# Kernel tuning notes

Measured on AMD Instinct MI355X. Metric: run time of the kernel, lower is better.

The kernel has to match this reference:

```python
import jax, jax.numpy as jnp
import numpy as np

B, T, E, H = 2, 2048, 1024, 16
D = E // H  # head_dim = 64


def setup_inputs() -> dict:
    key = jax.random.key(0)
    ks = jax.random.split(key, 9)
    s = 0.02
    x = jax.random.normal(ks[0], (B, T, E), dtype=jnp.float32)
    # additive causal mask, broadcastable to (B, H, T, T)
    causal = jnp.tril(jnp.ones((T, T), dtype=bool))
    uni_causal_mask = jnp.where(causal, 0.0, -1e9).astype(jnp.float32)[None, None]
    # torch Linear weights are (out_features, in_features); out = H*D, in = D
    Wq = jax.random.normal(ks[1], (H * D, D), dtype=jnp.float32) * s
    bq = jax.random.normal(ks[2], (H * D,), dtype=jnp.float32) * s
    Wk = jax.random.normal(ks[3], (H * D, D), dtype=jnp.float32) * s
    bk = jax.random.normal(ks[4], (H * D,), dtype=jnp.float32) * s
    Wv = jax.random.normal(ks[5], (H * D, D), dtype=jnp.float32) * s
    bv = jax.random.normal(ks[6], (H * D,), dtype=jnp.float32) * s
    Wp = jax.random.normal(ks[7], (E, E), dtype=jnp.float32) * s
    bp = jax.random.normal(ks[8], (E,), dtype=jnp.float32) * s
    return {"x": x, "uni_causal_mask": uni_causal_mask,
            "Wq": Wq, "bq": bq, "Wk": Wk, "bk": bk,
            "Wv": Wv, "bv": bv, "Wp": Wp, "bp": bp}


def _per_head_proj(xh, W, b):
    # xh: (B, T, H, D). Original code projects each head's D-dim slice with
    # Linear(D, H*D) and get_head_dim keeps only the diagonal block i for
    # head i, i.e. each head uses W[i*D:(i+1)*D, :] and b[i*D:(i+1)*D].
    W3 = W.reshape(H, D, D)  # (H, out D, in D)
    b2 = b.reshape(H, D)
    y = jnp.einsum('bthi,hoi->bhto', xh, W3) + b2[None, :, None, :]
    return y  # (B, H, T, D)


def reference(x, uni_causal_mask, Wq, bq, Wk, bk, Wv, bv, Wp, bp):
    b, t, e = x.shape
    xh = x.reshape(b, t, H, D)
    q = _per_head_proj(xh, Wq, bq)  # (B,H,T,D)
    k = _per_head_proj(xh, Wk, bk)
    v = _per_head_proj(xh, Wv, bv)
    scale = D ** (-0.5)
    attn = jnp.einsum('bhtd,bhsd->bhts', (q * scale).astype(jnp.float32),
                      k.astype(jnp.float32))
    attn = attn + uni_causal_mask
    attn = jax.nn.softmax(attn, axis=-1).astype(x.dtype)
    out = jnp.einsum('bhts,bhsd->bhtd', attn, v)
    out = out.transpose(0, 2, 1, 3).reshape(b, t, e)
    return out @ Wp.T + bp
```

## Files before the change

kernel.cpp:

```cpp
#include <hip/hip_runtime.h>

typedef __attribute__((ext_vector_type(4))) float f32x4;
typedef __attribute__((ext_vector_type(8))) __bf16 bf16x8;
typedef __attribute__((ext_vector_type(4))) unsigned short us4;
typedef __attribute__((ext_vector_type(8))) unsigned short us8;

#define DEVI static __device__ __forceinline__

constexpr int T_ = 2048, E_ = 1024, H_ = 16, D_ = 64;
#define QSCALE (0.125f * 1.44269504088896f)

DEVI unsigned short f2b(float f) {
  union { __bf16 b; unsigned short u; } c; c.b = (__bf16)f; return c.u;
}

DEVI unsigned pkw(float a, float b) {
  union { __bf16 h[2]; unsigned u; } c;
  c.h[0] = (__bf16)a; c.h[1] = (__bf16)b; return c.u;
}

#if __has_builtin(__builtin_amdgcn_exp2f)
DEVI float fexp2(float x) { return __builtin_amdgcn_exp2f(x); }
#else
DEVI float fexp2(float x) { return __expf(x * 0.69314718056f); }
#endif

DEVI f32x4 mfma16(bf16x8 a, bf16x8 b, f32x4 c) {
  return __builtin_amdgcn_mfma_f32_16x16x32_bf16(a, b, c, 0, 0, 0);
}

__launch_bounds__(256)
__global__ void wcvt_kernel(const float* __restrict__ Wq,
                            const float* __restrict__ Wk,
                            const float* __restrict__ Wv,
                            unsigned short* __restrict__ wqb,
                            unsigned short* __restrict__ wkb,
                            unsigned short* __restrict__ wvb)
{
  int blk = blockIdx.x;
  const float* src; unsigned short* dst; float s = 1.0f;
  if (blk < 64)       { src = Wq; dst = wqb; s = QSCALE; }
  else if (blk < 128) { src = Wk; dst = wkb; blk -= 64; }
  else                { src = Wv; dst = wvb; blk -= 128; }
  int i = blk * 256 + threadIdx.x;
  float4 v = *(const float4*)(src + (size_t)i * 4);
  us4 o; o[0] = f2b(v.x * s); o[1] = f2b(v.y * s); o[2] = f2b(v.z * s); o[3] = f2b(v.w * s);
  *(us4*)(dst + (size_t)i * 4) = o;
}

__launch_bounds__(256)
__global__ void wpcvt_kernel(const float* __restrict__ Wp,
                             unsigned short* __restrict__ wpb)
{
  int i = blockIdx.x * 256 + threadIdx.x;
  float4 v = *(const float4*)(Wp + (size_t)i * 4);
  us4 o; o[0] = f2b(v.x); o[1] = f2b(v.y); o[2] = f2b(v.z); o[3] = f2b(v.w);
  *(us4*)(wpb + (size_t)i * 4) = o;
}

__launch_bounds__(256)
__global__ void qkv_kernel(const float* __restrict__ x,
                           const unsigned short* __restrict__ wqb,
                           const float* __restrict__ bq,
                           const unsigned short* __restrict__ wkb,
                           const float* __restrict__ bk,
                           const unsigned short* __restrict__ wvb,
                           const float* __restrict__ bv,
                           unsigned short* __restrict__ qo,
                           unsigned short* __restrict__ ko,
                           unsigned short* __restrict__ vto)
{
  const int bh = blockIdx.x;
  const int b  = bh >> 4;
  const int h  = bh & (H_ - 1);
  const int t0 = blockIdx.y * 128;
  __shared__ unsigned short Xl[128][72];
  __shared__ unsigned short Wl[3][64][72];
  const int tid = threadIdx.x;

  #pragma unroll
  for (int p = 0; p < 8; ++p) {
    int idx = p * 256 + tid;
    int row = idx >> 4, c4 = idx & 15;
    float4 v = *(const float4*)(x + ((size_t)(b * T_ + t0 + row)) * E_ + h * 64 + c4 * 4);
    us4 o; o[0] = f2b(v.x); o[1] = f2b(v.y); o[2] = f2b(v.z); o[3] = f2b(v.w);
    *(us4*)&Xl[row][c4 * 4] = o;
  }
  {
    const unsigned short* wsrc0 = wqb + (size_t)h * 4096;
    const unsigned short* wsrc1 = wkb + (size_t)h * 4096;
    const unsigned short* wsrc2 = wvb + (size_t)h * 4096;
    #pragma unroll
    for (int p = 0; p < 2; ++p) {
      int idx = p * 256 + tid;
      int row = idx >> 3, c8 = (idx & 7) * 8;
      *(us8*)&Wl[0][row][c8] = *(const us8*)(wsrc0 + row * 64 + c8);
      *(us8*)&Wl[1][row][c8] = *(const us8*)(wsrc1 + row * 64 + c8);
      *(us8*)&Wl[2][row][c8] = *(const us8*)(wsrc2 + row * 64 + c8);
    }
  }
  __syncthreads();

  const int w = tid >> 6, lane = tid & 63, lo = lane & 15, g = lane >> 4;
  const int tl0 = w * 32;

  bf16x8 xb[2][2];
  #pragma unroll
  for (int tt = 0; tt < 2; ++tt)
    #pragma unroll
    for (int kd = 0; kd < 2; ++kd)
      xb[tt][kd] = *(const bf16x8*)&Xl[tl0 + tt * 16 + lo][kd * 32 + g * 8];

  #pragma unroll
  for (int tsel = 0; tsel < 2; ++tsel) {
    const float* bias = tsel ? bk : bq;
    unsigned short* outp = tsel ? ko : qo;
    const float bs = tsel ? 1.0f : QSCALE;
    #pragma unroll
    for (int ot = 0; ot < 4; ++ot) {
      bf16x8 a0 = *(const bf16x8*)&Wl[tsel][ot * 16 + lo][g * 8];
      bf16x8 a1 = *(const bf16x8*)&Wl[tsel][ot * 16 + lo][32 + g * 8];
      float4 bv4 = *(const float4*)(bias + h * 64 + ot * 16 + g * 4);
      float bb[4] = {bv4.x * bs, bv4.y * bs, bv4.z * bs, bv4.w * bs};
      #pragma unroll
      for (int tt = 0; tt < 2; ++tt) {
        f32x4 acc = {0.f, 0.f, 0.f, 0.f};
        acc = mfma16(a0, xb[tt][0], acc);
        acc = mfma16(a1, xb[tt][1], acc);
        int tg = t0 + tl0 + tt * 16 + lo;
        us4 pk;
        #pragma unroll
        for (int r = 0; r < 4; ++r) pk[r] = f2b(acc[r] + bb[r]);
        *(us4*)(outp + ((size_t)(bh * T_ + tg)) * 64 + ot * 16 + g * 4) = pk;
      }
    }
  }

  #pragma unroll
  for (int rt = 0; rt < 2; ++rt) {
    bf16x8 a0 = *(const bf16x8*)&Xl[tl0 + rt * 16 + lo][g * 8];
    bf16x8 a1 = *(const bf16x8*)&Xl[tl0 + rt * 16 + lo][32 + g * 8];
    #pragma unroll
    for (int ct = 0; ct < 4; ++ct) {
      bf16x8 b0 = *(const bf16x8*)&Wl[2][ct * 16 + lo][g * 8];
      bf16x8 b1 = *(const bf16x8*)&Wl[2][ct * 16 + lo][32 + g * 8];
      f32x4 acc = {0.f, 0.f, 0.f, 0.f};
      acc = mfma16(a0, b0, acc);
      acc = mfma16(a1, b1, acc);
      int d = ct * 16 + lo;
      float bvs = bv[h * 64 + d];
      int tg = t0 + tl0 + rt * 16 + g * 4;
      us4 pk;
      #pragma unroll
      for (int r = 0; r < 4; ++r) pk[r] = f2b(acc[r] + bvs);
      *(us4*)(vto + ((size_t)(bh * 64 + d)) * T_ + tg) = pk;
    }
  }
}

__launch_bounds__(256)
__global__ void flash_kernel(const unsigned short* __restrict__ q,
                             const unsigned short* __restrict__ kk_,
                             const unsigned short* __restrict__ vt,
                             unsigned short* __restrict__ ao)
{
  const int bh = blockIdx.x;
  const int b = bh >> 4, h = bh & 15;
  const int qt = 31 - blockIdx.y;
  const int t0 = qt * 64;
  __shared__ unsigned short Kl[2][64][64];
  __shared__ unsigned short Vl[3][64][64];
  const int tid = threadIdx.x, w = tid >> 6, lane = tid & 63, lo = lane & 15, g = lane >> 4;
  const int rs = lo & 7;

  const int srow = tid >> 3, sgi = tid & 7;
  const int khalf = (srow >> 2) & 1;
  const int gsrc = (srow >> 3) ^ (khalf << 1);
  const int prow = khalf * 16 + gsrc * 4 + (srow & 3);
  const int kkey = (sgi ^ (prow & 7)) * 8;
  const int vkey = (sgi ^ (srow & 7)) * 8;
  const unsigned short* kbase = kk_ + ((size_t)bh * T_ + srow) * 64 + sgi * 8;
  const unsigned short* vrow0 = vt + ((size_t)(bh * 64 + srow)) * T_;
  const unsigned short* vrow1 = vrow0 + (size_t)32 * T_;
  const int vco0 = sgi * 8;
  const int vco1 = ((sgi ^ 2) * 8) + 4;

  const int tw = t0 + w * 16;

  bf16x8 qf[2];
  const unsigned short* qb = q + ((size_t)(bh * T_ + tw + lo)) * 64;
  #pragma unroll
  for (int kd = 0; kd < 2; ++kd)
    qf[kd] = *(const bf16x8*)(qb + kd * 32 + g * 8);

  const int sb0 = g * 8, sb1 = ((g ^ 2) * 8) + 4;

  union { unsigned u[4]; bf16x8 v; } onec;
  onec.u[0] = onec.u[1] = onec.u[2] = onec.u[3] = 0x3f803f80u;
  const bf16x8 onesv = onec.v;

  float m_ = -1e30f;
  f32x4 zero4 = {0.f, 0.f, 0.f, 0.f};
  f32x4 lacc = zero4;
  f32x4 oacc[4];
  #pragma unroll
  for (int dt = 0; dt < 4; ++dt) oacc[dt] = zero4;

  const int nsteps = qt + 1;
  union u8c { us4 h[2]; us8 v; };
  us8 kr0 = *(const us8*)(kbase);
  us8 kr1 = *(const us8*)(kbase + 2048);
  u8c vr0, vr1;
  vr0.h[0] = *(const us4*)(vrow0 + vco0);
  vr0.h[1] = *(const us4*)(vrow0 + vco1);
  vr1.h[0] = *(const us4*)(vrow1 + vco0);
  vr1.h[1] = *(const us4*)(vrow1 + vco1);
  *(us8*)&Kl[0][prow][kkey] = kr0;
  *(us8*)&Kl[0][prow + 32][kkey] = kr1;
  *(us8*)&Vl[0][srow][vkey] = vr0.v;
  *(us8*)&Vl[0][srow + 32][vkey] = vr1.v;
  if (nsteps > 1) {
    kr0 = *(const us8*)(kbase + 4096);
    kr1 = *(const us8*)(kbase + 4096 + 2048);
    vr0.h[0] = *(const us4*)(vrow0 + 64 + vco0);
    vr0.h[1] = *(const us4*)(vrow0 + 64 + vco1);
    vr1.h[0] = *(const us4*)(vrow1 + 64 + vco0);
    vr1.h[1] = *(const us4*)(vrow1 + 64 + vco1);
  }
  __syncthreads();

  bf16x8 pb[2];
  int vprev = 0;

  for (int stp = 0; stp < nsteps; ++stp) {
    const int cur = stp & 1;
    us8 nk0, nk1;
    u8c nv0, nv1;
    const bool pf = (stp + 2 < nsteps);
    if (pf) {
      const size_t ko_ = (size_t)(stp + 2) * 4096;
      const int so = (stp + 2) * 64;
      nk0 = *(const us8*)(kbase + ko_);
      nk1 = *(const us8*)(kbase + ko_ + 2048);
      nv0.h[0] = *(const us4*)(vrow0 + so + vco0);
      nv0.h[1] = *(const us4*)(vrow0 + so + vco1);
      nv1.h[0] = *(const us4*)(vrow1 + so + vco0);
      nv1.h[1] = *(const us4*)(vrow1 + so + vco1);
    }
    f32x4 sacc[4];
    #pragma unroll
    for (int ss = 0; ss < 4; ++ss) sacc[ss] = zero4;
    __builtin_amdgcn_s_setprio(1);
    #pragma unroll
    for (int ss = 0; ss < 4; ++ss) {
      bf16x8 ka0 = *(const bf16x8*)&Kl[cur][ss * 16 + lo][(g ^ rs) * 8];
      bf16x8 ka1 = *(const bf16x8*)&Kl[cur][ss * 16 + lo][((g | 4) ^ rs) * 8];
      sacc[ss] = mfma16(ka0, qf[0], sacc[ss]);
      sacc[ss] = mfma16(ka1, qf[1], sacc[ss]);
    }
    if (stp > 0) {
      #pragma unroll
      for (int kh = 0; kh < 2; ++kh) {
        #pragma unroll
        for (int dt = 0; dt < 4; ++dt) {
          bf16x8 va = *(const bf16x8*)&Vl[vprev][dt * 16 + lo][((kh * 4 + g) ^ rs) * 8];
          oacc[dt] = mfma16(va, pb[kh], oacc[dt]);
        }
      }
    }
    __builtin_amdgcn_s_setprio(0);
    if (stp == nsteps - 1) {
      #pragma unroll
      for (int ss = 0; ss < 4; ++ss) {
        const int sb = ((ss & 1) ? sb1 : sb0) + (ss >> 1) * 32;
        #pragma unroll
        for (int r = 0; r < 4; ++r) {
          if (t0 + sb + r > tw + lo) sacc[ss][r] = -1e30f;
        }
      }
    }
    float mx = -1e30f;
    #pragma unroll
    for (int ss = 0; ss < 4; ++ss) {
      float a = fmaxf(sacc[ss][0], sacc[ss][1]);
      float c = fmaxf(sacc[ss][2], sacc[ss][3]);
      mx = fmaxf(mx, fmaxf(a, c));
    }
    if (!__all(mx <= m_ + 8.0f)) {
      mx = fmaxf(mx, __shfl_xor(mx, 16));
      mx = fmaxf(mx, __shfl_xor(mx, 32));
      float mn = fmaxf(m_, mx);
      float corr = fexp2(m_ - mn);
      m_ = mn;
      lacc *= corr;
      #pragma unroll
      for (int dt = 0; dt < 4; ++dt) oacc[dt] *= corr;
    }
    #pragma unroll
    for (int kh = 0; kh < 2; ++kh) {
      union { unsigned u[4]; bf16x8 v; } pbc;
      #pragma unroll
      for (int half2 = 0; half2 < 2; ++half2) {
        const int ss = kh * 2 + half2;
        float p0 = fexp2(sacc[ss][0] - m_);
        float p1 = fexp2(sacc[ss][1] - m_);
        float p2 = fexp2(sacc[ss][2] - m_);
        float p3 = fexp2(sacc[ss][3] - m_);
        pbc.u[half2 * 2]     = pkw(p0, p1);
        pbc.u[half2 * 2 + 1] = pkw(p2, p3);
      }
      pb[kh] = pbc.v;
      lacc = mfma16(onesv, pb[kh], lacc);
    }
    vprev = stp % 3;
    if (stp + 1 < nsteps) {
      *(us8*)&Kl[cur ^ 1][prow][kkey] = kr0;
      *(us8*)&Kl[cur ^ 1][prow + 32][kkey] = kr1;
      const int vn = (stp + 1) % 3;
      *(us8*)&Vl[vn][srow][vkey] = vr0.v;
      *(us8*)&Vl[vn][srow + 32][vkey] = vr1.v;
    }
    __syncthreads();
    if (pf) { kr0 = nk0; kr1 = nk1; vr0 = nv0; vr1 = nv1; }
  }
  __builtin_amdgcn_s_setprio(1);
  #pragma unroll
  for (int kh = 0; kh < 2; ++kh) {
    #pragma unroll
    for (int dt = 0; dt < 4; ++dt) {
      bf16x8 va = *(const bf16x8*)&Vl[vprev][dt * 16 + lo][((kh * 4 + g) ^ rs) * 8];
      oacc[dt] = mfma16(va, pb[kh], oacc[dt]);
    }
  }
  __builtin_amdgcn_s_setprio(0);
  float inv = 1.0f / lacc[0];
  unsigned short* op = ao + ((size_t)(b * T_ + tw + lo)) * E_ + h * 64;
  #pragma unroll
  for (int dt = 0; dt < 4; ++dt) {
    us4 pk;
    #pragma unroll
    for (int r = 0; r < 4; ++r) pk[r] = f2b(oacc[dt][r] * inv);
    *(us4*)(op + dt * 16 + g * 4) = pk;
  }
}

__launch_bounds__(256)
__global__ void proj_kernel(const unsigned short* __restrict__ ao,
                            const unsigned short* __restrict__ wpb,
                            const float* __restrict__ bp,
                            float* __restrict__ out)
{
  const int bid = blockIdx.x;
  const int xcd = bid & 7, idx = bid >> 3;
  const int m0 = (xcd * 4 + (idx & 3)) * 128;
  const int n0 = (idx >> 2) * 64;
  __shared__ unsigned short Al[2][128][40];
  __shared__ unsigned short Bl[2][64][40];
  const int tid = threadIdx.x, w = tid >> 6, lane = tid & 63, lo = lane & 15, g = lane >> 4;
  const int wr = (w >> 1) * 64, wc = (w & 1) * 32;
  f32x4 zero4 = {0.f, 0.f, 0.f, 0.f};
  f32x4 acc[4][2];
  #pragma unroll
  for (int i = 0; i < 4; ++i)
    #pragma unroll
    for (int j = 0; j < 2; ++j) acc[i][j] = zero4;

  const int arow = tid >> 1, acol = (tid & 1) * 16;
  const int brow = tid >> 2, bcol = (tid & 3) * 8;
  const unsigned short* abase = ao + (size_t)(m0 + arow) * 1024 + acol;
  const unsigned short* bbase = wpb + (size_t)(n0 + brow) * 1024 + bcol;

  us8 a0 = *(const us8*)(abase);
  us8 a1 = *(const us8*)(abase + 8);
  us8 b0 = *(const us8*)(bbase);
  *(us8*)&Al[0][arow][acol] = a0;
  *(us8*)&Al[0][arow][acol + 8] = a1;
  *(us8*)&Bl[0][brow][bcol] = b0;
  a0 = *(const us8*)(abase + 32);
  a1 = *(const us8*)(abase + 40);
  b0 = *(const us8*)(bbase + 32);
  __syncthreads();

  for (int it = 0; it < 32; ++it) {
    const int cur = it & 1;
    us8 na0, na1, nb0;
    const bool pf = (it + 2 < 32);
    if (pf) {
      const int kn = (it + 2) * 32;
      na0 = *(const us8*)(abase + kn);
      na1 = *(const us8*)(abase + kn + 8);
      nb0 = *(const us8*)(bbase + kn);
    }
    bf16x8 af[4], bfr[2];
    #pragma unroll
    for (int i = 0; i < 4; ++i) af[i] = *(const bf16x8*)&Al[cur][wr + i * 16 + lo][g * 8];
    #pragma unroll
    for (int j = 0; j < 2; ++j) bfr[j] = *(const bf16x8*)&Bl[cur][wc + j * 16 + lo][g * 8];
    __builtin_amdgcn_s_setprio(1);
    #pragma unroll
    for (int i = 0; i < 4; ++i)
      #pragma unroll
      for (int j = 0; j < 2; ++j)
        acc[i][j] = mfma16(af[i], bfr[j], acc[i][j]);
    __builtin_amdgcn_s_setprio(0);
    if (it + 1 < 32) {
      *(us8*)&Al[cur ^ 1][arow][acol] = a0;
      *(us8*)&Al[cur ^ 1][arow][acol + 8] = a1;
      *(us8*)&Bl[cur ^ 1][brow][bcol] = b0;
    }
    __syncthreads();
    if (pf) { a0 = na0; a1 = na1; b0 = nb0; }
  }
  #pragma unroll
  for (int j = 0; j < 2; ++j) {
    int n = n0 + wc + j * 16 + lo;
    float bias = bp[n];
    #pragma unroll
    for (int i = 0; i < 4; ++i) {
      #pragma unroll
      for (int r = 0; r < 4; ++r)
        out[(size_t)(m0 + wr + i * 16 + g * 4 + r) * 1024 + n] = acc[i][j][r] + bias;
    }
  }
}

extern "C" void kernel_launch(void* const* d_in, const int* in_sizes, int n_in,
                              void* d_out, int out_size, void* d_ws, size_t ws_size,
                              hipStream_t stream)
{
  const float* x  = (const float*)d_in[0];
  const float* Wq = (const float*)d_in[2];
  const float* bq = (const float*)d_in[3];
  const float* Wk = (const float*)d_in[4];
  const float* bk = (const float*)d_in[5];
  const float* Wv = (const float*)d_in[6];
  const float* bv = (const float*)d_in[7];
  const float* Wp = (const float*)d_in[8];
  const float* bp = (const float*)d_in[9];
  float* out = (float*)d_out;

  char* ws = (char*)d_ws;
  const size_t SZ = (size_t)2 * 16 * 2048 * 64 * 2;
  unsigned short* q  = (unsigned short*)(ws);
  unsigned short* kb = (unsigned short*)(ws + SZ);
  unsigned short* vt = (unsigned short*)(ws + 2 * SZ);
  unsigned short* ao = (unsigned short*)(ws + 3 * SZ);
  unsigned short* wqb = ao;
  unsigned short* wkb = ao + 65536;
  unsigned short* wvb = ao + 131072;
  unsigned short* wpb = q;

  wcvt_kernel<<<dim3(192), 256, 0, stream>>>(Wq, Wk, Wv, wqb, wkb, wvb);
  qkv_kernel<<<dim3(32, 16), 256, 0, stream>>>(x, wqb, bq, wkb, bk, wvb, bv, q, kb, vt);
  flash_kernel<<<dim3(32, 32), 256, 0, stream>>>(q, kb, vt, ao);
  wpcvt_kernel<<<dim3(1024), 256, 0, stream>>>(Wp, wpb);
  proj_kernel<<<dim3(512), 256, 0, stream>>>(ao, wpb, bp, out);
}
```

Measured before the change: 79.81 us.

## Enlarge flash attention query tile to 128 rows, two 16-row subtiles per wave

Each flash block now handles 128 query rows instead of 64, with every wave processing two 16-row query subtiles against the same K/V tiles loaded into shared memory. This halves the K/V global loads and LDS staging per query row and gives each wave more independent MFMA work per synchronization. In exchange the grid shrinks from 1024 to 512 blocks, register pressure roughly doubles for the accumulators, and the causal mask is now applied per step on the diagonal region, so occupancy and load balance may suffer.

```diff
diff --git a/kernel.cpp b/kernel.cpp
--- a/kernel.cpp
+++ b/kernel.cpp
@@ -166,8 +166,8 @@
 {
   const int bh = blockIdx.x;
   const int b = bh >> 4, h = bh & 15;
-  const int qt = 31 - blockIdx.y;
-  const int t0 = qt * 64;
+  const int qt = 15 - blockIdx.y;
+  const int t0 = qt * 128;
   __shared__ unsigned short Kl[2][64][64];
   __shared__ unsigned short Vl[3][64][64];
   const int tid = threadIdx.x, w = tid >> 6, lane = tid & 63, lo = lane & 15, g = lane >> 4;
@@ -185,13 +185,16 @@
   const int vco0 = sgi * 8;
   const int vco1 = ((sgi ^ 2) * 8) + 4;
 
-  const int tw = t0 + w * 16;
-
-  bf16x8 qf[2];
-  const unsigned short* qb = q + ((size_t)(bh * T_ + tw + lo)) * 64;
-  #pragma unroll
-  for (int kd = 0; kd < 2; ++kd)
-    qf[kd] = *(const bf16x8*)(qb + kd * 32 + g * 8);
+  const int tw = t0 + w * 32;
+
+  bf16x8 qf[2][2];
+  #pragma unroll
+  for (int tt = 0; tt < 2; ++tt) {
+    const unsigned short* qb = q + ((size_t)(bh * T_ + tw + tt * 16 + lo)) * 64;
+    #pragma unroll
+    for (int kd = 0; kd < 2; ++kd)
+      qf[tt][kd] = *(const bf16x8*)(qb + kd * 32 + g * 8);
+  }
 
   const int sb0 = g * 8, sb1 = ((g ^ 2) * 8) + 4;
 
@@ -199,14 +202,16 @@
   onec.u[0] = onec.u[1] = onec.u[2] = onec.u[3] = 0x3f803f80u;
   const bf16x8 onesv = onec.v;
 
-  float m_ = -1e30f;
+  float m_[2] = {-1e30f, -1e30f};
   f32x4 zero4 = {0.f, 0.f, 0.f, 0.f};
-  f32x4 lacc = zero4;
-  f32x4 oacc[4];
-  #pragma unroll
-  for (int dt = 0; dt < 4; ++dt) oacc[dt] = zero4;
-
-  const int nsteps = qt + 1;
+  f32x4 lacc[2] = {zero4, zero4};
+  f32x4 oacc[4][2];
+  #pragma unroll
+  for (int dt = 0; dt < 4; ++dt)
+    #pragma unroll
+    for (int tt = 0; tt < 2; ++tt) oacc[dt][tt] = zero4;
+
+  const int nsteps = 2 * qt + 2;
   union u8c { us4 h[2]; us8 v; };
   us8 kr0 = *(const us8*)(kbase);
   us8 kr1 = *(const us8*)(kbase + 2048);
@@ -219,20 +224,19 @@
   *(us8*)&Kl[0][prow + 32][kkey] = kr1;
   *(us8*)&Vl[0][srow][vkey] = vr0.v;
   *(us8*)&Vl[0][srow + 32][vkey] = vr1.v;
-  if (nsteps > 1) {
-    kr0 = *(const us8*)(kbase + 4096);
-    kr1 = *(const us8*)(kbase + 4096 + 2048);
-    vr0.h[0] = *(const us4*)(vrow0 + 64 + vco0);
-    vr0.h[1] = *(const us4*)(vrow0 + 64 + vco1);
-    vr1.h[0] = *(const us4*)(vrow1 + 64 + vco0);
-    vr1.h[1] = *(const us4*)(vrow1 + 64 + vco1);
-  }
+  kr0 = *(const us8*)(kbase + 4096);
+  kr1 = *(const us8*)(kbase + 4096 + 2048);
+  vr0.h[0] = *(const us4*)(vrow0 + 64 + vco0);
+  vr0.h[1] = *(const us4*)(vrow0 + 64 + vco1);
+  vr1.h[0] = *(const us4*)(vrow1 + 64 + vco0);
+  vr1.h[1] = *(const us4*)(vrow1 + 64 + vco1);
   __syncthreads();
 
-  bf16x8 pb[2];
+  bf16x8 pb[2][2];
   int vprev = 0;
 
   for (int stp = 0; stp < nsteps; ++stp) {
+    const int s0 = stp * 64;
     const int cur = stp & 1;
     us8 nk0, nk1;
     u8c nv0, nv1;
@@ -247,16 +251,21 @@
       nv1.h[0] = *(const us4*)(vrow1 + so + vco0);
       nv1.h[1] = *(const us4*)(vrow1 + so + vco1);
     }
-    f32x4 sacc[4];
-    #pragma unroll
-    for (int ss = 0; ss < 4; ++ss) sacc[ss] = zero4;
+    f32x4 sacc[4][2];
+    #pragma unroll
+    for (int ss = 0; ss < 4; ++ss)
+      #pragma unroll
+      for (int tt = 0; tt < 2; ++tt) sacc[ss][tt] = zero4;
     __builtin_amdgcn_s_setprio(1);
     #pragma unroll
     for (int ss = 0; ss < 4; ++ss) {
       bf16x8 ka0 = *(const bf16x8*)&Kl[cur][ss * 16 + lo][(g ^ rs) * 8];
       bf16x8 ka1 = *(const bf16x8*)&Kl[cur][ss * 16 + lo][((g | 4) ^ rs) * 8];
-      sacc[ss] = mfma16(ka0, qf[0], sacc[ss]);
-      sacc[ss] = mfma16(ka1, qf[1], sacc[ss]);
+      #pragma unroll
+      for (int tt = 0; tt < 2; ++tt) {
+        sacc[ss][tt] = mfma16(ka0, qf[tt][0], sacc[ss][tt]);
+        sacc[ss][tt] = mfma16(ka1, qf[tt][1], sacc[ss][tt]);
+      }
     }
     if (stp > 0) {
       #pragma unroll
@@ -264,53 +273,68 @@
         #pragma unroll
         for (int dt = 0; dt < 4; ++dt) {
           bf16x8 va = *(const bf16x8*)&Vl[vprev][dt * 16 + lo][((kh * 4 + g) ^ rs) * 8];
-          oacc[dt] = mfma16(va, pb[kh], oacc[dt]);
+          #pragma unroll
+          for (int tt = 0; tt < 2; ++tt)
+            oacc[dt][tt] = mfma16(va, pb[tt][kh], oacc[dt][tt]);
         }
       }
     }
     __builtin_amdgcn_s_setprio(0);
-    if (stp == nsteps - 1) {
+    if (s0 + 63 > tw) {
       #pragma unroll
       for (int ss = 0; ss < 4; ++ss) {
-        const int sb = ((ss & 1) ? sb1 : sb0) + (ss >> 1) * 32;
+        const int sb = s0 + ((ss & 1) ? sb1 : sb0) + (ss >> 1) * 32;
         #pragma unroll
-        for (int r = 0; r < 4; ++r) {
-          if (t0 + sb + r > tw + lo) sacc[ss][r] = -1e30f;
+        for (int tt = 0; tt < 2; ++tt) {
+          const int tg = tw + tt * 16 + lo;
+          #pragma unroll
+          for (int r = 0; r < 4; ++r) {
+            if (sb + r > tg) sacc[ss][tt][r] = -1e30f;
+          }
         }
       }
     }
-    float mx = -1e30f;
-    #pragma unroll
-    for (int ss = 0; ss < 4; ++ss) {
-      float a = fmaxf(sacc[ss][0], sacc[ss][1]);
-      float c = fmaxf(sacc[ss][2], sacc[ss][3]);
-      mx = fmaxf(mx, fmaxf(a, c));
-    }
-    if (!__all(mx <= m_ + 8.0f)) {
-      mx = fmaxf(mx, __shfl_xor(mx, 16));
-      mx = fmaxf(mx, __shfl_xor(mx, 32));
-      float mn = fmaxf(m_, mx);
-      float corr = fexp2(m_ - mn);
-      m_ = mn;
-      lacc *= corr;
-      #pragma unroll
-      for (int dt = 0; dt < 4; ++dt) oacc[dt] *= corr;
-    }
-    #pragma unroll
-    for (int kh = 0; kh < 2; ++kh) {
-      union { unsigned u[4]; bf16x8 v; } pbc;
-      #pragma unroll
-      for (int half2 = 0; half2 < 2; ++half2) {
-        const int ss = kh * 2 + half2;
-        float p0 = fexp2(sacc[ss][0] - m_);
-        float p1 = fexp2(sacc[ss][1] - m_);
-        float p2 = fexp2(sacc[ss][2] - m_);
-        float p3 = fexp2(sacc[ss][3] - m_);
-        pbc.u[half2 * 2]     = pkw(p0, p1);
-        pbc.u[half2 * 2 + 1] = pkw(p2, p3);
-      }
-      pb[kh] = pbc.v;
-      lacc = mfma16(onesv, pb[kh], lacc);
+    float mx[2];
+    #pragma unroll
+    for (int tt = 0; tt < 2; ++tt) {
+      float a = fmaxf(fmaxf(sacc[0][tt][0], sacc[0][tt][1]), fmaxf(sacc[0][tt][2], sacc[0][tt][3]));
+      float b2 = fmaxf(fmaxf(sacc[1][tt][0], sacc[1][tt][1]), fmaxf(sacc[1][tt][2], sacc[1][tt][3]));
+      float c = fmaxf(fmaxf(sacc[2][tt][0], sacc[2][tt][1]), fmaxf(sacc[2][tt][2], sacc[2][tt][3]));
+      float d = fmaxf(fmaxf(sacc[3][tt][0], sacc[3][tt][1]), fmaxf(sacc[3][tt][2], sacc[3][tt][3]));
+      mx[tt] = fmaxf(fmaxf(a, b2), fmaxf(c, d));
+    }
+    if (!__all((mx[0] <= m_[0] + 8.0f) && (mx[1] <= m_[1] + 8.0f))) {
+      #pragma unroll
+      for (int tt = 0; tt < 2; ++tt) {
+        float mv = mx[tt];
+        mv = fmaxf(mv, __shfl_xor(mv, 16));
+        mv = fmaxf(mv, __shfl_xor(mv, 32));
+        float mn = fmaxf(m_[tt], mv);
+        float corr = fexp2(m_[tt] - mn);
+        m_[tt] = mn;
+        lacc[tt] *= corr;
+        #pragma unroll
+        for (int dt = 0; dt < 4; ++dt) oacc[dt][tt] *= corr;
+      }
+    }
+    #pragma unroll
+    for (int tt = 0; tt < 2; ++tt) {
+      #pragma unroll
+      for (int kh = 0; kh < 2; ++kh) {
+        union { unsigned u[4]; bf16x8 v; } pbc;
+        #pragma unroll
+        for (int half2 = 0; half2 < 2; ++half2) {
+          const int ss = kh * 2 + half2;
+          float p0 = fexp2(sacc[ss][tt][0] - m_[tt]);
+          float p1 = fexp2(sacc[ss][tt][1] - m_[tt]);
+          float p2 = fexp2(sacc[ss][tt][2] - m_[tt]);
+          float p3 = fexp2(sacc[ss][tt][3] - m_[tt]);
+          pbc.u[half2 * 2]     = pkw(p0, p1);
+          pbc.u[half2 * 2 + 1] = pkw(p2, p3);
+        }
+        pb[tt][kh] = pbc.v;
+        lacc[tt] = mfma16(onesv, pb[tt][kh], lacc[tt]);
+      }
     }
     vprev = stp % 3;
     if (stp + 1 < nsteps) {
@@ -329,18 +353,23 @@
     #pragma unroll
     for (int dt = 0; dt < 4; ++dt) {
       bf16x8 va = *(const bf16x8*)&Vl[vprev][dt * 16 + lo][((kh * 4 + g) ^ rs) * 8];
-      oacc[dt] = mfma16(va, pb[kh], oacc[dt]);
+      #pragma unroll
+      for (int tt = 0; tt < 2; ++tt)
+        oacc[dt][tt] = mfma16(va, pb[tt][kh], oacc[dt][tt]);
     }
   }
   __builtin_amdgcn_s_setprio(0);
-  float inv = 1.0f / lacc[0];
-  unsigned short* op = ao + ((size_t)(b * T_ + tw + lo)) * E_ + h * 64;
-  #pragma unroll
-  for (int dt = 0; dt < 4; ++dt) {
-    us4 pk;
-    #pragma unroll
-    for (int r = 0; r < 4; ++r) pk[r] = f2b(oacc[dt][r] * inv);
-    *(us4*)(op + dt * 16 + g * 4) = pk;
+  #pragma unroll
+  for (int tt = 0; tt < 2; ++tt) {
+    float inv = 1.0f / lacc[tt][0];
+    unsigned short* op = ao + ((size_t)(b * T_ + tw + tt * 16 + lo)) * E_ + h * 64;
+    #pragma unroll
+    for (int dt = 0; dt < 4; ++dt) {
+      us4 pk;
+      #pragma unroll
+      for (int r = 0; r < 4; ++r) pk[r] = f2b(oacc[dt][tt][r] * inv);
+      *(us4*)(op + dt * 16 + g * 4) = pk;
+    }
   }
 }
 
@@ -452,7 +481,7 @@
 
   wcvt_kernel<<<dim3(192), 256, 0, stream>>>(Wq, Wk, Wv, wqb, wkb, wvb);
   qkv_kernel<<<dim3(32, 16), 256, 0, stream>>>(x, wqb, bq, wkb, bk, wvb, bv, q, kb, vt);
-  flash_kernel<<<dim3(32, 32), 256, 0, stream>>>(q, kb, vt, ao);
+  flash_kernel<<<dim3(32, 16), 256, 0, stream>>>(q, kb, vt, ao);
   wpcvt_kernel<<<dim3(1024), 256, 0, stream>>>(Wp, wpb);
   proj_kernel<<<dim3(512), 256, 0, stream>>>(ao, wpb, bp, out);
 }
```

New measurement: 88.42 us. +10.8%, slower.

## Split long causal query tiles across two KV halves and merge partials

Applied to the files above, without the earlier changes.

The flash attention kernel becomes a flattened 1536-block grid. The 16 longest query tiles per head are each split into two blocks that process halves of the KV range and write unnormalized fp32 partial outputs plus (max, sum) pairs. A new merge kernel combines the halves with log-sum-exp rescaling. This is meant to balance the causal triangle workload and shorten the tail on long tiles, at the cost of extra fp32 partial traffic and an additional kernel launch.

```diff
diff --git a/kernel.cpp b/kernel.cpp
--- a/kernel.cpp
+++ b/kernel.cpp
@@ -162,11 +162,31 @@
 __global__ void flash_kernel(const unsigned short* __restrict__ q,
                              const unsigned short* __restrict__ kk_,
                              const unsigned short* __restrict__ vt,
-                             unsigned short* __restrict__ ao)
-{
-  const int bh = blockIdx.x;
+                             unsigned short* __restrict__ ao,
+                             float* __restrict__ opart,
+                             float2* __restrict__ mlb)
+{
+  const int id = blockIdx.x;
+  int bh, qt, hf, sfirst, scount;
+  bool split;
+  if (id < 1024) {
+    const int sq = id >> 5;
+    bh = id & 31;
+    qt = 31 - (sq >> 1);
+    hf = sq & 1;
+    const int tot = qt + 1;
+    const int nl = (tot + 1) >> 1;
+    if (hf == 0) { sfirst = 0; scount = nl; }
+    else         { sfirst = nl; scount = tot - nl; }
+    split = true;
+  } else {
+    const int j = id - 1024;
+    bh = j & 31;
+    qt = 15 - (j >> 5);
+    hf = 0; sfirst = 0; scount = qt + 1;
+    split = false;
+  }
   const int b = bh >> 4, h = bh & 15;
-  const int qt = 31 - blockIdx.y;
   const int t0 = qt * 64;
   __shared__ unsigned short Kl[2][64][64];
   __shared__ unsigned short Vl[3][64][64];
@@ -179,8 +199,9 @@
   const int prow = khalf * 16 + gsrc * 4 + (srow & 3);
   const int kkey = (sgi ^ (prow & 7)) * 8;
   const int vkey = (sgi ^ (srow & 7)) * 8;
-  const unsigned short* kbase = kk_ + ((size_t)bh * T_ + srow) * 64 + sgi * 8;
-  const unsigned short* vrow0 = vt + ((size_t)(bh * 64 + srow)) * T_;
+  const unsigned short* kbase = kk_ + ((size_t)bh * T_ + srow) * 64 + sgi * 8
+                                + (size_t)sfirst * 4096;
+  const unsigned short* vrow0 = vt + ((size_t)(bh * 64 + srow)) * T_ + sfirst * 64;
   const unsigned short* vrow1 = vrow0 + (size_t)32 * T_;
   const int vco0 = sgi * 8;
   const int vco1 = ((sgi ^ 2) * 8) + 4;
@@ -206,46 +227,46 @@
   #pragma unroll
   for (int dt = 0; dt < 4; ++dt) oacc[dt] = zero4;
 
-  const int nsteps = qt + 1;
-  union u8c { us4 h[2]; us8 v; };
+  union u8c { us4 h4[2]; us8 v; };
   us8 kr0 = *(const us8*)(kbase);
   us8 kr1 = *(const us8*)(kbase + 2048);
   u8c vr0, vr1;
-  vr0.h[0] = *(const us4*)(vrow0 + vco0);
-  vr0.h[1] = *(const us4*)(vrow0 + vco1);
-  vr1.h[0] = *(const us4*)(vrow1 + vco0);
-  vr1.h[1] = *(const us4*)(vrow1 + vco1);
+  vr0.h4[0] = *(const us4*)(vrow0 + vco0);
+  vr0.h4[1] = *(const us4*)(vrow0 + vco1);
+  vr1.h4[0] = *(const us4*)(vrow1 + vco0);
+  vr1.h4[1] = *(const us4*)(vrow1 + vco1);
   *(us8*)&Kl[0][prow][kkey] = kr0;
   *(us8*)&Kl[0][prow + 32][kkey] = kr1;
   *(us8*)&Vl[0][srow][vkey] = vr0.v;
   *(us8*)&Vl[0][srow + 32][vkey] = vr1.v;
-  if (nsteps > 1) {
+  if (scount > 1) {
     kr0 = *(const us8*)(kbase + 4096);
     kr1 = *(const us8*)(kbase + 4096 + 2048);
-    vr0.h[0] = *(const us4*)(vrow0 + 64 + vco0);
-    vr0.h[1] = *(const us4*)(vrow0 + 64 + vco1);
-    vr1.h[0] = *(const us4*)(vrow1 + 64 + vco0);
-    vr1.h[1] = *(const us4*)(vrow1 + 64 + vco1);
+    vr0.h4[0] = *(const us4*)(vrow0 + 64 + vco0);
+    vr0.h4[1] = *(const us4*)(vrow0 + 64 + vco1);
+    vr1.h4[0] = *(const us4*)(vrow1 + 64 + vco0);
+    vr1.h4[1] = *(const us4*)(vrow1 + 64 + vco1);
   }
   __syncthreads();
 
   bf16x8 pb[2];
   int vprev = 0;
 
-  for (int stp = 0; stp < nsteps; ++stp) {
+  for (int stp = 0; stp < scount; ++stp) {
     const int cur = stp & 1;
+    const int s0 = (sfirst + stp) * 64;
     us8 nk0, nk1;
     u8c nv0, nv1;
-    const bool pf = (stp + 2 < nsteps);
+    const bool pf = (stp + 2 < scount);
     if (pf) {
       const size_t ko_ = (size_t)(stp + 2) * 4096;
       const int so = (stp + 2) * 64;
       nk0 = *(const us8*)(kbase + ko_);
       nk1 = *(const us8*)(kbase + ko_ + 2048);
-      nv0.h[0] = *(const us4*)(vrow0 + so + vco0);
-      nv0.h[1] = *(const us4*)(vrow0 + so + vco1);
-      nv1.h[0] = *(const us4*)(vrow1 + so + vco0);
-      nv1.h[1] = *(const us4*)(vrow1 + so + vco1);
+      nv0.h4[0] = *(const us4*)(vrow0 + so + vco0);
+      nv0.h4[1] = *(const us4*)(vrow0 + so + vco1);
+      nv1.h4[0] = *(const us4*)(vrow1 + so + vco0);
+      nv1.h4[1] = *(const us4*)(vrow1 + so + vco1);
     }
     f32x4 sacc[4];
     #pragma unroll
@@ -269,13 +290,13 @@
       }
     }
     __builtin_amdgcn_s_setprio(0);
-    if (stp == nsteps - 1) {
+    if (s0 + 63 > tw) {
       #pragma unroll
       for (int ss = 0; ss < 4; ++ss) {
-        const int sb = ((ss & 1) ? sb1 : sb0) + (ss >> 1) * 32;
+        const int sb = s0 + ((ss & 1) ? sb1 : sb0) + (ss >> 1) * 32;
         #pragma unroll
         for (int r = 0; r < 4; ++r) {
-          if (t0 + sb + r > tw + lo) sacc[ss][r] = -1e30f;
+          if (sb + r > tw + lo) sacc[ss][r] = -1e30f;
         }
       }
     }
@@ -313,7 +334,7 @@
       lacc = mfma16(onesv, pb[kh], lacc);
     }
     vprev = stp % 3;
-    if (stp + 1 < nsteps) {
+    if (stp + 1 < scount) {
       *(us8*)&Kl[cur ^ 1][prow][kkey] = kr0;
       *(us8*)&Kl[cur ^ 1][prow + 32][kkey] = kr1;
       const int vn = (stp + 1) % 3;
@@ -333,15 +354,53 @@
     }
   }
   __builtin_amdgcn_s_setprio(0);
-  float inv = 1.0f / lacc[0];
-  unsigned short* op = ao + ((size_t)(b * T_ + tw + lo)) * E_ + h * 64;
-  #pragma unroll
-  for (int dt = 0; dt < 4; ++dt) {
-    us4 pk;
-    #pragma unroll
-    for (int r = 0; r < 4; ++r) pk[r] = f2b(oacc[dt][r] * inv);
-    *(us4*)(op + dt * 16 + g * 4) = pk;
-  }
+  if (split) {
+    const int tr = tw + lo - 1024;
+    float* ob = opart + (((size_t)(hf * 32 + bh) * 1024 + tr)) * 64;
+    #pragma unroll
+    for (int dt = 0; dt < 4; ++dt) {
+      float4 o4; o4.x = oacc[dt][0]; o4.y = oacc[dt][1];
+      o4.z = oacc[dt][2]; o4.w = oacc[dt][3];
+      *(float4*)(ob + dt * 16 + g * 4) = o4;
+    }
+    if (g == 0)
+      mlb[(size_t)(hf * 32 + bh) * 1024 + tr] = make_float2(m_, lacc[0]);
+  } else {
+    float inv = 1.0f / lacc[0];
+    unsigned short* op = ao + ((size_t)(b * T_ + tw + lo)) * E_ + h * 64;
+    #pragma unroll
+    for (int dt = 0; dt < 4; ++dt) {
+      us4 pk;
+      #pragma unroll
+      for (int r = 0; r < 4; ++r) pk[r] = f2b(oacc[dt][r] * inv);
+      *(us4*)(op + dt * 16 + g * 4) = pk;
+    }
+  }
+}
+
+__launch_bounds__(256)
+__global__ void merge_kernel(const float* __restrict__ opart,
+                             const float2* __restrict__ mlb,
+                             unsigned short* __restrict__ ao)
+{
+  const int u = blockIdx.x * 256 + threadIdx.x;
+  const int dchunk = u & 15;
+  const int tr = (u >> 4) & 1023;
+  const int bh = u >> 14;
+  const int b = bh >> 4, h = bh & 15;
+  float2 ml0 = mlb[(size_t)bh * 1024 + tr];
+  float2 ml1 = mlb[(size_t)(32 + bh) * 1024 + tr];
+  float m = fmaxf(ml0.x, ml1.x);
+  float w0 = fexp2(ml0.x - m), w1 = fexp2(ml1.x - m);
+  float inv = 1.0f / (ml0.y * w0 + ml1.y * w1);
+  float4 a = *(const float4*)(opart + ((size_t)bh * 1024 + tr) * 64 + dchunk * 4);
+  float4 c = *(const float4*)(opart + ((size_t)(32 + bh) * 1024 + tr) * 64 + dchunk * 4);
+  us4 pk;
+  pk[0] = f2b((a.x * w0 + c.x * w1) * inv);
+  pk[1] = f2b((a.y * w0 + c.y * w1) * inv);
+  pk[2] = f2b((a.z * w0 + c.z * w1) * inv);
+  pk[3] = f2b((a.w * w0 + c.w * w1) * inv);
+  *(us4*)(ao + ((size_t)(b * T_ + 1024 + tr)) * E_ + h * 64 + dchunk * 4) = pk;
 }
 
 __launch_bounds__(256)
@@ -445,6 +504,8 @@
   unsigned short* kb = (unsigned short*)(ws + SZ);
   unsigned short* vt = (unsigned short*)(ws + 2 * SZ);
   unsigned short* ao = (unsigned short*)(ws + 3 * SZ);
+  float* opart = (float*)(ws + 4 * SZ);
+  float2* mlb  = (float2*)(ws + 4 * SZ + (size_t)16 * 1024 * 1024);
   unsigned short* wqb = ao;
   unsigned short* wkb = ao + 65536;
   unsigned short* wvb = ao + 131072;
@@ -452,7 +513,8 @@
 
   wcvt_kernel<<<dim3(192), 256, 0, stream>>>(Wq, Wk, Wv, wqb, wkb, wvb);
   qkv_kernel<<<dim3(32, 16), 256, 0, stream>>>(x, wqb, bq, wkb, bk, wvb, bv, q, kb, vt);
-  flash_kernel<<<dim3(32, 32), 256, 0, stream>>>(q, kb, vt, ao);
+  flash_kernel<<<dim3(1536), 256, 0, stream>>>(q, kb, vt, ao, opart, mlb);
+  merge_kernel<<<dim3(2048), 256, 0, stream>>>(opart, mlb, ao);
   wpcvt_kernel<<<dim3(1024), 256, 0, stream>>>(Wp, wpb);
   proj_kernel<<<dim3(512), 256, 0, stream>>>(ao, wpb, bp, out);
 }
```

Result: slower. 85.35 us (+6.9%).
